# Kernel optimization log

Hardware: AMD Instinct MI355X
Metric: run time of the kernel (lower is better)

Reference implementation:

```python
import jax, jax.numpy as jnp
import numpy as np

N_EMBD = 768
N_HEAD = 12
HEAD_DIM = N_EMBD // N_HEAD


def setup_inputs() -> dict:
    key = jax.random.key(0)
    ks = jax.random.split(key, 5)
    B, T, C = 1, 4096, N_EMBD
    s = 1.0 / np.sqrt(C)
    return {
        "x": jax.random.normal(ks[0], (B, T, C), dtype=jnp.float32),
        "wq": jax.random.normal(ks[1], (C, C), dtype=jnp.float32) * s,
        "wk": jax.random.normal(ks[2], (C, C), dtype=jnp.float32) * s,
        "wv": jax.random.normal(ks[3], (C, C), dtype=jnp.float32) * s,
        "wo": jax.random.normal(ks[4], (C, C), dtype=jnp.float32) * s,
    }


def reference(x, wq, wk, wv, wo):
    B, T, C = x.shape
    H, D = N_HEAD, HEAD_DIM
    # projections: torch Linear(y = x @ W^T); weights stored as (out, in)
    q = (x @ wq.T).reshape(B, T, H, D).transpose(0, 2, 1, 3)  # B H T D
    k = (x @ wk.T).reshape(B, T, H, D).transpose(0, 2, 1, 3)
    v = (x @ wv.T).reshape(B, T, H, D).transpose(0, 2, 1, 3)
    scale = 1.0 / jnp.sqrt(jnp.asarray(D, dtype=x.dtype))
    attn = jnp.einsum("bhtd,bhsd->bhts", q, k) * scale  # B H T T
    causal = jnp.tril(jnp.ones((T, T), dtype=bool))
    attn = jnp.where(causal, attn, -jnp.inf)
    attn = jax.nn.softmax(attn, axis=-1)
    out = jnp.einsum("bhts,bhsd->bhtd", attn, v)  # B H T D
    out = out.transpose(0, 2, 1, 3).reshape(B, T, C)
    return out @ wo.T
```

## Files before the change

### kernel.cpp

```cpp
#include <hip/hip_runtime.h>


#define T_SEQ 4096
#define C_EMB 768
#define NH    12
#define HD    64

typedef __attribute__((ext_vector_type(8))) short bf16x8;
typedef __attribute__((ext_vector_type(4))) float floatx4;

#define QSCALE 0.18033688011112042f

__device__ __forceinline__ unsigned short f2bf(float f) {
  union { float f; unsigned u; } v; v.f = f;
  unsigned r = v.u + 0x7fffu + ((v.u >> 16) & 1u);
  return (unsigned short)(r >> 16);
}
__device__ __forceinline__ unsigned short f2bf_rhu(float f) {
  union { float f; unsigned u; } v; v.f = f;
  return (unsigned short)((v.u + 0x8000u) >> 16);
}
__device__ __forceinline__ float bf2f(unsigned short h) {
  union { unsigned u; float f; } v; v.u = ((unsigned)h) << 16;
  return v.f;
}

__device__ __forceinline__ void gload_lds16(const void* gptr, void* ldsptr) {
  __builtin_amdgcn_global_load_lds(
      (const __attribute__((address_space(1))) unsigned int*)gptr,
      (__attribute__((address_space(3))) unsigned int*)ldsptr,
      16, 0, 0);
}

__global__ void cast_all_kernel(const float* __restrict__ x,
                                const float* __restrict__ wq,
                                const float* __restrict__ wk,
                                const float* __restrict__ wv,
                                const float* __restrict__ wo,
                                unsigned short* __restrict__ dst) {
  const int GX = (T_SEQ * C_EMB) / 4;
  const int GW = (C_EMB * C_EMB) / 4;
  int i = blockIdx.x * blockDim.x + threadIdx.x;
  const float* src; int local;
  if (i < GX) { src = x; local = i; }
  else {
    int t = i - GX; int w = t / GW; local = t - w * GW;
    src = (w == 0) ? wq : (w == 1) ? wk : (w == 2) ? wv : wo;
  }
  float4 f = reinterpret_cast<const float4*>(src)[local];
  ushort4 u;
  u.x = f2bf(f.x); u.y = f2bf(f.y); u.z = f2bf(f.z); u.w = f2bf(f.w);
  reinterpret_cast<ushort4*>(dst)[i] = u;
}

__global__ __launch_bounds__(256) void gemm_qkv(
    const unsigned short* __restrict__ A,
    const unsigned short* __restrict__ B,
    unsigned short* __restrict__ Qb,
    unsigned short* __restrict__ Kb,
    unsigned short* __restrict__ Vt) {
  constexpr int K = 768, BM = 64, BN = 128, BK = 64;
  __shared__ __align__(16) unsigned short As0[BM * BK];
  __shared__ __align__(16) unsigned short Bs0[BN * BK];
  __shared__ __align__(16) unsigned short As1[BM * BK];
  __shared__ __align__(16) unsigned short Bs1[BN * BK];
  const int tid = threadIdx.x;
  const int wave = tid >> 6, lane = tid & 63;
  const int lm = lane & 15, lq = lane >> 4;
  const int swz = lm & 7;
  const int m0 = blockIdx.x * BM, n0 = blockIdx.y * BN;
  const int wm = (wave & 1) * 32, wn = (wave >> 1) * 64;
  floatx4 acc[2][4] = {};

  auto stage = [&](int k0, unsigned short* Ad, unsigned short* Bd) {
#pragma unroll
    for (int i = 0; i < 2; i++) {
      int idx = i * 256 + tid;
      int row = idx >> 3;
      int ch = (idx & 7) ^ (row & 7);
      gload_lds16(A + (size_t)(m0 + row) * K + k0 + ch * 8, (char*)Ad + idx * 16);
    }
#pragma unroll
    for (int i = 0; i < 4; i++) {
      int idx = i * 256 + tid;
      int row = idx >> 3;
      int ch = (idx & 7) ^ (row & 7);
      gload_lds16(B + (size_t)(n0 + row) * K + k0 + ch * 8, (char*)Bd + idx * 16);
    }
  };

  auto compute = [&](const unsigned short* Asb, const unsigned short* Bsb) {
#pragma unroll
    for (int kk = 0; kk < 2; kk++) {
      bf16x8 af[2], bfr[4];
#pragma unroll
      for (int i = 0; i < 2; i++) {
        int row = wm + i * 16 + lm;
        af[i] = *(const bf16x8*)(Asb + row * BK + (((kk * 4 + lq) ^ swz) * 8));
      }
#pragma unroll
      for (int j = 0; j < 4; j++) {
        int row = wn + j * 16 + lm;
        bfr[j] = *(const bf16x8*)(Bsb + row * BK + (((kk * 4 + lq) ^ swz) * 8));
      }
#pragma unroll
      for (int i = 0; i < 2; i++)
#pragma unroll
        for (int j = 0; j < 4; j++)
          acc[i][j] = __builtin_amdgcn_mfma_f32_16x16x32_bf16(af[i], bfr[j], acc[i][j], 0, 0, 0);
    }
  };

  stage(0, As0, Bs0);
  int k0 = 0;
  while (true) {
    __syncthreads();
    if (k0 + BK < K) stage(k0 + BK, As1, Bs1);
    compute(As0, Bs0);
    k0 += BK; if (k0 >= K) break;
    __syncthreads();
    if (k0 + BK < K) stage(k0 + BK, As0, Bs0);
    compute(As1, Bs1);
    k0 += BK; if (k0 >= K) break;
  }

  const int which = n0 / C_EMB;
  if (which < 2) {
    unsigned short* tgt = (which == 0) ? Qb : Kb;
    const float sc = (which == 0) ? QSCALE : 1.0f;
#pragma unroll
    for (int i = 0; i < 2; i++)
#pragma unroll
      for (int j = 0; j < 4; j++) {
        int n = n0 - which * C_EMB + wn + j * 16 + lm;
        int h = n >> 6, d = n & 63;
#pragma unroll
        for (int r = 0; r < 4; r++) {
          int m = m0 + wm + i * 16 + lq * 4 + r;
          tgt[(((size_t)h * T_SEQ + m) << 6) + d] = f2bf(acc[i][j][r] * sc);
        }
      }
  } else {
#pragma unroll
    for (int i = 0; i < 2; i++)
#pragma unroll
      for (int j = 0; j < 4; j++) {
        int n = n0 - 2 * C_EMB + wn + j * 16 + lm;
        int h = n >> 6, d = n & 63;
        int m = m0 + wm + i * 16 + lq * 4;
        ushort4 pk;
        pk.x = f2bf(acc[i][j][0]); pk.y = f2bf(acc[i][j][1]);
        pk.z = f2bf(acc[i][j][2]); pk.w = f2bf(acc[i][j][3]);
        *(ushort4*)(Vt + ((size_t)(h * HD + d)) * T_SEQ + m) = pk;
      }
  }
}

struct AttnState {
  float rsum[2][4];
  floatx4 o_acc[2][4];
};

template <typename EpilogueFn>
__device__ __forceinline__ void attn_body(
    const unsigned short* __restrict__ Q,
    const unsigned short* __restrict__ K,
    const unsigned short* __restrict__ Vt,
    int h, int q0, int sb, int se,
    EpilogueFn epi) {
  constexpr int BS = 64, PS = 72, KVB = BS * HD;
  __shared__ __align__(16) unsigned short Ks0[KVB];
  __shared__ __align__(16) unsigned short Vs0[KVB];
  __shared__ __align__(16) unsigned short Ks1[KVB];
  __shared__ __align__(16) unsigned short Vs1[KVB];
  __shared__ __align__(16) unsigned short Ps[4 * 32 * PS];

  const int tid = threadIdx.x;
  const int wave = tid >> 6, lane = tid & 63;
  const int lm = lane & 15, lq = lane >> 4;
  const unsigned short* Qh = Q + (size_t)h * T_SEQ * HD;
  const unsigned short* Kh = K + (size_t)h * T_SEQ * HD;
  const unsigned short* Vh = Vt + (size_t)h * HD * T_SEQ;
  const int qrow_base = q0 + wave * 32;
  unsigned short* Pw = Ps + wave * 32 * PS;
  const int swz = lm & 7;

  bf16x8 qf[2][2];
#pragma unroll
  for (int m = 0; m < 2; m++)
#pragma unroll
    for (int kk = 0; kk < 2; kk++)
      qf[m][kk] = *(const bf16x8*)(Qh + (size_t)(qrow_base + m * 16 + lm) * HD + kk * 32 + lq * 8);

  AttnState st;
#pragma unroll
  for (int m = 0; m < 2; m++)
#pragma unroll
    for (int r = 0; r < 4; r++) { st.rsum[m][r] = 0.f; st.o_acc[m][r] = floatx4{0.f,0.f,0.f,0.f}; }

  auto stage = [&](int s0, unsigned short* Kd, unsigned short* Vd) {
#pragma unroll
    for (int i = 0; i < 2; i++) {
      int idx = (wave * 2 + i) * 64 + lane;
      int row = idx >> 3;
      int ch = (idx & 7) ^ (row & 7);
      gload_lds16(Kh + (size_t)(s0 + row) * HD + ch * 8, (char*)Kd + idx * 16);
      gload_lds16(Vh + (size_t)row * T_SEQ + s0 + ch * 8, (char*)Vd + idx * 16);
    }
  };

  auto compute = [&](int it, const unsigned short* Kc, const unsigned short* Vc) {
    const int s0 = it * BS;
    floatx4 sa[2][4] = {};
#pragma unroll
    for (int kk = 0; kk < 2; kk++)
#pragma unroll
      for (int j = 0; j < 4; j++) {
        int row = j * 16 + lm;
        bf16x8 kf = *(const bf16x8*)(Kc + (row * 8 + ((kk * 4 + lq) ^ swz)) * 8);
#pragma unroll
        for (int m = 0; m < 2; m++)
          sa[m][j] = __builtin_amdgcn_mfma_f32_16x16x32_bf16(qf[m][kk], kf, sa[m][j], 0, 0, 0);
      }

    if (s0 >= q0) {
#pragma unroll
      for (int m = 0; m < 2; m++)
#pragma unroll
        for (int j = 0; j < 4; j++) {
          int scol = s0 + j * 16 + lm;
#pragma unroll
          for (int r = 0; r < 4; r++) {
            int qrow = qrow_base + m * 16 + lq * 4 + r;
            if (scol > qrow) sa[m][j][r] = -1e30f;
          }
        }
    }

#pragma unroll
    for (int m = 0; m < 2; m++)
#pragma unroll
      for (int j = 0; j < 4; j++)
#pragma unroll
        for (int r = 0; r < 4; r++) {
          float p = __builtin_amdgcn_exp2f(sa[m][j][r]);
          st.rsum[m][r] += p;
          Pw[(m * 16 + lq * 4 + r) * PS + j * 16 + lm] = f2bf_rhu(p);
        }

#pragma unroll
    for (int kk = 0; kk < 2; kk++) {
      bf16x8 pf[2];
#pragma unroll
      for (int m = 0; m < 2; m++)
        pf[m] = *(const bf16x8*)(Pw + (m * 16 + lm) * PS + kk * 32 + lq * 8);
#pragma unroll
      for (int jd = 0; jd < 4; jd++) {
        int row = jd * 16 + lm;
        bf16x8 vf = *(const bf16x8*)(Vc + (row * 8 + ((kk * 4 + lq) ^ swz)) * 8);
#pragma unroll
        for (int m = 0; m < 2; m++)
          st.o_acc[m][jd] = __builtin_amdgcn_mfma_f32_16x16x32_bf16(pf[m], vf, st.o_acc[m][jd], 0, 0, 0);
      }
    }
  };

  stage(sb * BS, Ks0, Vs0);
  int it = sb;
  while (true) {
    __syncthreads();
    if (it + 1 < se) stage((it + 1) * BS, Ks1, Vs1);
    compute(it, Ks0, Vs0);
    if (++it >= se) break;
    __syncthreads();
    if (it + 1 < se) stage((it + 1) * BS, Ks0, Vs0);
    compute(it, Ks1, Vs1);
    if (++it >= se) break;
  }

#pragma unroll
  for (int m = 0; m < 2; m++)
#pragma unroll
    for (int r = 0; r < 4; r++) {
      float s = st.rsum[m][r];
      s += __shfl_xor(s, 1);
      s += __shfl_xor(s, 2);
      s += __shfl_xor(s, 4);
      s += __shfl_xor(s, 8);
      st.rsum[m][r] = s;
    }
  epi(st, qrow_base, lm, lq);
}

__global__ __launch_bounds__(256, 3) void attn_kernelA(
    const unsigned short* __restrict__ Q,
    const unsigned short* __restrict__ K,
    const unsigned short* __restrict__ Vt,
    float* __restrict__ Opart,
    float* __restrict__ lpart) {
  const int bid = blockIdx.x;
  const int h = bid % NH;
  const int z = bid / NH;
  const int qt = (T_SEQ / 128 - 1) - (z >> 1);
  const int c = z & 1;
  const int q0 = qt * 128;
  const int sb = c ? (qt + 1) : 0;
  const int se = c ? (2 * qt + 2) : (qt + 1);

  const size_t CN = (size_t)NH * T_SEQ * HD;
  float* Oc = Opart + (size_t)c * CN;
  float* lc = lpart + (size_t)c * NH * T_SEQ;
  attn_body(Q, K, Vt, h, q0, sb, se,
    [&](const AttnState& st, int qrow_base, int lm, int lq) {
#pragma unroll
      for (int m = 0; m < 2; m++)
#pragma unroll
        for (int r = 0; r < 4; r++) {
          int t = qrow_base + m * 16 + lq * 4 + r;
          if (lm == 0) lc[h * T_SEQ + t] = st.rsum[m][r];
#pragma unroll
          for (int jd = 0; jd < 4; jd++)
            Oc[((size_t)h * T_SEQ + t) * HD + jd * 16 + lm] = st.o_acc[m][jd][r];
        }
    });
}

__global__ void combine_kernelA(const float* __restrict__ Opart,
                                const float* __restrict__ lpart,
                                unsigned short* __restrict__ Ob) {
  int idx = blockIdx.x * blockDim.x + threadIdx.x;
  int d4 = idx & 15;
  int t = (idx >> 4) & (T_SEQ - 1);
  int h = idx >> 16;
  const size_t CN4 = (size_t)NH * T_SEQ * HD / 4;
  float4 a = reinterpret_cast<const float4*>(Opart)[idx];
  float4 b = reinterpret_cast<const float4*>(Opart)[CN4 + idx];
  float l = lpart[h * T_SEQ + t] + lpart[NH * T_SEQ + h * T_SEQ + t];
  float inv = 1.0f / l;
  ushort4 u;
  u.x = f2bf((a.x + b.x) * inv); u.y = f2bf((a.y + b.y) * inv);
  u.z = f2bf((a.z + b.z) * inv); u.w = f2bf((a.w + b.w) * inv);
  *(ushort4*)(Ob + (size_t)t * C_EMB + h * HD + d4 * 4) = u;
}

__global__ __launch_bounds__(256, 3) void attn_kernel2(
    const unsigned short* __restrict__ Q,
    const unsigned short* __restrict__ K,
    const unsigned short* __restrict__ Vt,
    unsigned short* __restrict__ Op0,
    unsigned short* __restrict__ Op1,
    float* __restrict__ lpart) {
  const int bid = blockIdx.x;
  const int h = bid % NH;
  const int z = bid / NH;
  const int qt = (T_SEQ / 128 - 1) - (z >> 1);
  const int c = z & 1;
  const int q0 = qt * 128;
  const int sb = c ? (qt + 1) : 0;
  const int se = c ? (2 * qt + 2) : (qt + 1);

  unsigned short* Oc = c ? Op1 : Op0;
  float* lc = lpart + (size_t)c * NH * T_SEQ;
  attn_body(Q, K, Vt, h, q0, sb, se,
    [&](const AttnState& st, int qrow_base, int lm, int lq) {
#pragma unroll
      for (int m = 0; m < 2; m++)
#pragma unroll
        for (int r = 0; r < 4; r++) {
          int t = qrow_base + m * 16 + lq * 4 + r;
          if (lm == 0) lc[h * T_SEQ + t] = st.rsum[m][r];
#pragma unroll
          for (int jd = 0; jd < 4; jd++)
            Oc[((size_t)h * T_SEQ + t) * HD + jd * 16 + lm] = f2bf(st.o_acc[m][jd][r]);
        }
    });
}

__global__ void combine_kernel2(const unsigned short* __restrict__ Op0,
                                const unsigned short* __restrict__ Op1,
                                const float* __restrict__ lpart,
                                unsigned short* __restrict__ Ob) {
  int idx = blockIdx.x * blockDim.x + threadIdx.x;
  int d4 = idx & 15;
  int t = (idx >> 4) & (T_SEQ - 1);
  int h = idx >> 16;
  float l = lpart[h * T_SEQ + t] + lpart[NH * T_SEQ + h * T_SEQ + t];
  float inv = 1.0f / l;
  ushort4 a = reinterpret_cast<const ushort4*>(Op0)[idx];
  ushort4 b = reinterpret_cast<const ushort4*>(Op1)[idx];
  ushort4 u;
  u.x = f2bf((bf2f(a.x) + bf2f(b.x)) * inv);
  u.y = f2bf((bf2f(a.y) + bf2f(b.y)) * inv);
  u.z = f2bf((bf2f(a.z) + bf2f(b.z)) * inv);
  u.w = f2bf((bf2f(a.w) + bf2f(b.w)) * inv);
  *(ushort4*)(Ob + (size_t)t * C_EMB + h * HD + d4 * 4) = u;
}

__global__ __launch_bounds__(256) void gemm_out(
    const unsigned short* __restrict__ A,
    const unsigned short* __restrict__ B,
    float* __restrict__ Out) {
  constexpr int K = 768, BM = 64, BN = 128, BK = 64;
  __shared__ __align__(16) unsigned short As0[BM * BK];
  __shared__ __align__(16) unsigned short Bs0[BN * BK];
  __shared__ __align__(16) unsigned short As1[BM * BK];
  __shared__ __align__(16) unsigned short Bs1[BN * BK];
  const int tid = threadIdx.x;
  const int wave = tid >> 6, lane = tid & 63;
  const int lm = lane & 15, lq = lane >> 4;
  const int swz = lm & 7;
  const int m0 = blockIdx.x * BM, n0 = blockIdx.y * BN;
  const int wm = (wave & 1) * 32, wn = (wave >> 1) * 64;
  floatx4 acc[2][4] = {};

  auto stage = [&](int k0, unsigned short* Ad, unsigned short* Bd) {
#pragma unroll
    for (int i = 0; i < 2; i++) {
      int idx = i * 256 + tid;
      int row = idx >> 3;
      int ch = (idx & 7) ^ (row & 7);
      gload_lds16(A + (size_t)(m0 + row) * K + k0 + ch * 8, (char*)Ad + idx * 16);
    }
#pragma unroll
    for (int i = 0; i < 4; i++) {
      int idx = i * 256 + tid;
      int row = idx >> 3;
      int ch = (idx & 7) ^ (row & 7);
      gload_lds16(B + (size_t)(n0 + row) * K + k0 + ch * 8, (char*)Bd + idx * 16);
    }
  };

  auto compute = [&](const unsigned short* Asb, const unsigned short* Bsb) {
#pragma unroll
    for (int kk = 0; kk < 2; kk++) {
      bf16x8 af[2], bfr[4];
#pragma unroll
      for (int i = 0; i < 2; i++) {
        int row = wm + i * 16 + lm;
        af[i] = *(const bf16x8*)(Asb + row * BK + (((kk * 4 + lq) ^ swz) * 8));
      }
#pragma unroll
      for (int j = 0; j < 4; j++) {
        int row = wn + j * 16 + lm;
        bfr[j] = *(const bf16x8*)(Bsb + row * BK + (((kk * 4 + lq) ^ swz) * 8));
      }
#pragma unroll
      for (int i = 0; i < 2; i++)
#pragma unroll
        for (int j = 0; j < 4; j++)
          acc[i][j] = __builtin_amdgcn_mfma_f32_16x16x32_bf16(af[i], bfr[j], acc[i][j], 0, 0, 0);
    }
  };

  stage(0, As0, Bs0);
  int k0 = 0;
  while (true) {
    __syncthreads();
    if (k0 + BK < K) stage(k0 + BK, As1, Bs1);
    compute(As0, Bs0);
    k0 += BK; if (k0 >= K) break;
    __syncthreads();
    if (k0 + BK < K) stage(k0 + BK, As0, Bs0);
    compute(As1, Bs1);
    k0 += BK; if (k0 >= K) break;
  }

#pragma unroll
  for (int i = 0; i < 2; i++)
#pragma unroll
    for (int j = 0; j < 4; j++)
#pragma unroll
      for (int r = 0; r < 4; r++) {
        int m = m0 + wm + i * 16 + lq * 4 + r;
        int n = n0 + wn + j * 16 + lm;
        Out[(size_t)m * C_EMB + n] = acc[i][j][r];
      }
}

extern "C" void kernel_launch(void* const* d_in, const int* in_sizes, int n_in,
                              void* d_out, int out_size, void* d_ws, size_t ws_size,
                              hipStream_t stream) {
  const float* x  = (const float*)d_in[0];
  const float* wq = (const float*)d_in[1];
  const float* wk = (const float*)d_in[2];
  const float* wv = (const float*)d_in[3];
  const float* wo = (const float*)d_in[4];
  float* out = (float*)d_out;

  const size_t XN = (size_t)T_SEQ * C_EMB;
  const size_t WN = (size_t)C_EMB * C_EMB;
  unsigned short* base = (unsigned short*)d_ws;

  unsigned short* Xb   = base;
  unsigned short* Wqkv = base + XN;
  unsigned short* Wob  = base + XN + 3 * WN;
  unsigned short* Qb   = base + XN + 4 * WN;
  unsigned short* Kb   = Qb + XN;
  unsigned short* Vt   = Kb + XN;
  unsigned short* tail = Vt + XN;
  unsigned short* Ob   = Qb;

  const size_t needA = 29884416ull + 2ull * XN * 4ull + 2ull * NH * T_SEQ * 4ull;

  const int ngroups = (int)((XN + 4 * WN) / 4);
  cast_all_kernel<<<dim3(ngroups / 256), 256, 0, stream>>>(x, wq, wk, wv, wo, Xb);

  gemm_qkv<<<dim3(T_SEQ / 64, 2304 / 128), 256, 0, stream>>>(Xb, Wqkv, Qb, Kb, Vt);

  if (ws_size >= needA) {
    float* OpartA = (float*)tail;
    float* lpartA = OpartA + 2 * XN;
    attn_kernelA<<<dim3((T_SEQ / 128) * 2 * NH), 256, 0, stream>>>(Qb, Kb, Vt, OpartA, lpartA);
    combine_kernelA<<<dim3((int)(XN / 4) / 256), 256, 0, stream>>>(OpartA, lpartA, Ob);
  } else {
    unsigned short* Op0 = base;
    unsigned short* Op1 = tail;
    float* lpart = (float*)(base + XN);
    attn_kernel2<<<dim3((T_SEQ / 128) * 2 * NH), 256, 0, stream>>>(Qb, Kb, Vt, Op0, Op1, lpart);
    combine_kernel2<<<dim3((int)(XN / 4) / 256), 256, 0, stream>>>(Op0, Op1, lpart, Ob);
  }

  gemm_out<<<dim3(T_SEQ / 64, C_EMB / 128), 256, 0, stream>>>(Ob, Wob, out);
}
```

Measured before the change: 162.4 us.

## Software-pipeline PV MFMA one tile behind QK in attention loop

Restructures the attention inner loop so the P·V matrix multiply for the previous key block is issued after the current block's QK^T MFMAs. P and V fragments are loaded into registers at the end of each phase and consumed in the next. The aim is to overlap the exp/softmax and LDS traffic with independent MFMA work. It raises register pressure (pfp/vfp held across iterations), which could hurt occupancy under launch_bounds(256,3).

After: 294.6 us. 1.81x slower.

```diff
diff --git a/kernel.cpp b/kernel.cpp
--- a/kernel.cpp
+++ b/kernel.cpp
@@ -198,6 +198,9 @@
 #pragma unroll
     for (int r = 0; r < 4; r++) { st.rsum[m][r] = 0.f; st.o_acc[m][r] = floatx4{0.f,0.f,0.f,0.f}; }
 
+  bf16x8 pfp[2][2];
+  bf16x8 vfp[2][4];
+
   auto stage = [&](int s0, unsigned short* Kd, unsigned short* Vd) {
 #pragma unroll
     for (int i = 0; i < 2; i++) {
@@ -209,7 +212,17 @@
     }
   };
 
-  auto compute = [&](int it, const unsigned short* Kc, const unsigned short* Vc) {
+  auto pv_prev = [&]() {
+#pragma unroll
+    for (int kk = 0; kk < 2; kk++)
+#pragma unroll
+      for (int jd = 0; jd < 4; jd++)
+#pragma unroll
+        for (int m = 0; m < 2; m++)
+          st.o_acc[m][jd] = __builtin_amdgcn_mfma_f32_16x16x32_bf16(pfp[m][kk], vfp[kk][jd], st.o_acc[m][jd], 0, 0, 0);
+  };
+
+  auto phase = [&](int it, const unsigned short* Kc, const unsigned short* Vc, bool do_pv) {
     const int s0 = it * BS;
     floatx4 sa[2][4] = {};
 #pragma unroll
@@ -222,6 +235,8 @@
         for (int m = 0; m < 2; m++)
           sa[m][j] = __builtin_amdgcn_mfma_f32_16x16x32_bf16(qf[m][kk], kf, sa[m][j], 0, 0, 0);
       }
+
+    if (do_pv) pv_prev();
 
     if (s0 >= q0) {
 #pragma unroll
@@ -249,34 +264,38 @@
         }
 
 #pragma unroll
-    for (int kk = 0; kk < 2; kk++) {
-      bf16x8 pf[2];
+    for (int kk = 0; kk < 2; kk++)
 #pragma unroll
       for (int m = 0; m < 2; m++)
-        pf[m] = *(const bf16x8*)(Pw + (m * 16 + lm) * PS + kk * 32 + lq * 8);
+        pfp[m][kk] = *(const bf16x8*)(Pw + (m * 16 + lm) * PS + kk * 32 + lq * 8);
+#pragma unroll
+    for (int kk = 0; kk < 2; kk++)
 #pragma unroll
       for (int jd = 0; jd < 4; jd++) {
         int row = jd * 16 + lm;
-        bf16x8 vf = *(const bf16x8*)(Vc + (row * 8 + ((kk * 4 + lq) ^ swz)) * 8);
-#pragma unroll
-        for (int m = 0; m < 2; m++)
-          st.o_acc[m][jd] = __builtin_amdgcn_mfma_f32_16x16x32_bf16(pf[m], vf, st.o_acc[m][jd], 0, 0, 0);
-      }
-    }
+        vfp[kk][jd] = *(const bf16x8*)(Vc + (row * 8 + ((kk * 4 + lq) ^ swz)) * 8);
+      }
   };
 
   stage(sb * BS, Ks0, Vs0);
   int it = sb;
-  while (true) {
-    __syncthreads();
-    if (it + 1 < se) stage((it + 1) * BS, Ks1, Vs1);
-    compute(it, Ks0, Vs0);
-    if (++it >= se) break;
-    __syncthreads();
-    if (it + 1 < se) stage((it + 1) * BS, Ks0, Vs0);
-    compute(it, Ks1, Vs1);
-    if (++it >= se) break;
+  __syncthreads();
+  if (it + 1 < se) stage((it + 1) * BS, Ks1, Vs1);
+  phase(it, Ks0, Vs0, false);
+  ++it;
+  if (it < se) {
+    while (true) {
+      __syncthreads();
+      if (it + 1 < se) stage((it + 1) * BS, Ks0, Vs0);
+      phase(it, Ks1, Vs1, true);
+      if (++it >= se) break;
+      __syncthreads();
+      if (it + 1 < se) stage((it + 1) * BS, Ks1, Vs1);
+      phase(it, Ks0, Vs0, true);
+      if (++it >= se) break;
+    }
   }
+  pv_prev();
 
 #pragma unroll
   for (int m = 0; m < 2; m++)
```
